# Kernel optimization log

Measured on AMD Instinct MI355X. Metric: run time of the kernel, lower is better.

## Reference

```python
import jax, jax.numpy as jnp
import numpy as np
import math

B, CIN, H, W = 32, 128, 64, 64
COUT, KH, KW = 256, 3, 3


def setup_inputs() -> dict:
    key = jax.random.key(0)
    k1, k2, k3 = jax.random.split(key, 3)
    sqrtk = math.sqrt(1.0 / (CIN * KH * KW))
    x = jax.random.normal(k1, (B, CIN, H, W), dtype=jnp.float32)
    weight = jax.random.uniform(k2, (COUT, CIN, KH, KW), dtype=jnp.float32, minval=-sqrtk, maxval=sqrtk)
    bias = jax.random.uniform(k3, (COUT,), dtype=jnp.float32, minval=-sqrtk, maxval=sqrtk)
    return {"input": x, "weight": weight, "bias": bias}


def reference(input, weight, bias):
    # VALID (no padding), stride-1 cross-correlation conv, NCHW/OIHW layout,
    # matching the original nested-loop direct convolution + per-channel bias.
    out = jax.lax.conv_general_dilated(
        input, weight,
        window_strides=(1, 1), padding='VALID',
        dimension_numbers=('NCHW', 'OIHW', 'NCHW'))
    return out + bias[None, :, None, None]
```

## Files before the change

kernel.cpp:

```cpp
#include <hip/hip_runtime.h>

#define NB   32
#define NCI  128
#define NH   64
#define NW   64
#define NCO  256
#define NOH  62
#define NOW  62

typedef __attribute__((ext_vector_type(8))) short bf16x8;
typedef __attribute__((ext_vector_type(8))) unsigned short u16x8;
typedef __attribute__((ext_vector_type(4))) float f32x4;

typedef __attribute__((address_space(1))) const unsigned int glb_u32_t;
typedef __attribute__((address_space(3))) unsigned int lds_u32_t;

__device__ __forceinline__ unsigned short f2bf(float f) {
  unsigned int u = __float_as_uint(f);
  u = u + 0x7FFFu + ((u >> 16) & 1u);
  return (unsigned short)(u >> 16);
}

__device__ __forceinline__ void gload_lds16(const unsigned short* g, unsigned short* l) {
  __builtin_amdgcn_global_load_lds((glb_u32_t*)g, (lds_u32_t*)l, 16, 0, 0);
}

__global__ __launch_bounds__(256) void cvt_x_kernel(const float* __restrict__ x,
                                                    unsigned short* __restrict__ xt) {
  __shared__ unsigned short l[64 * 130];
  const int tid = threadIdx.x;
  const int b = blockIdx.x >> 6, h = blockIdx.x & 63;
  const int w0 = tid & 63, c0 = tid >> 6;
  const float* src = x + ((size_t)b * NCI * NH + h) * NW;
  #pragma unroll
  for (int g = 0; g < 32; ++g) {
    int ci = g * 4 + c0;
    l[w0 * 130 + ci] = f2bf(src[(size_t)ci * (NH * NW) + w0]);
  }
  __syncthreads();
  unsigned short* dst = xt + ((size_t)b * NH + h) * NW * NCI;
  #pragma unroll
  for (int it = 0; it < 4; ++it) {
    int gidx = it * 2048 + tid * 8;
    int w = gidx >> 7, ci0 = gidx & 127;
    const unsigned int* lw = (const unsigned int*)(l + w * 130 + ci0);
    union { u16x8 v; unsigned int u[4]; } t;
    t.u[0] = lw[0]; t.u[1] = lw[1]; t.u[2] = lw[2]; t.u[3] = lw[3];
    *(u16x8*)(dst + w * NCI + ci0) = t.v;
  }
}

__global__ __launch_bounds__(256) void cvt_w_kernel(const float* __restrict__ wsrc,
                                                    unsigned short* __restrict__ wt) {
  int t = blockIdx.x * 256 + threadIdx.x;
  int oc = t & 15, co = (t >> 4) & 255, k = t >> 12;
  const float* src = wsrc + ((size_t)co * NCI + oc * 8) * 9 + k;
  u16x8 v;
  #pragma unroll
  for (int j = 0; j < 8; ++j) v[j] = f2bf(src[j * 9]);
  *(u16x8*)(wt + ((size_t)k * NCO + co) * NCI + oc * 8) = v;
}

__global__ __launch_bounds__(256, 2) void conv_mfma_kernel(
    const unsigned short* __restrict__ xt, const unsigned short* __restrict__ wt,
    const float* __restrict__ bias, float* __restrict__ out) {
  __shared__ unsigned short smem[40960];

  const int tid  = threadIdx.x;
  const int lane = tid & 63;
  const int wid  = tid >> 6;
  const int wn   = wid;
  const int l15  = lane & 15;
  const int lo   = lane >> 4;

  const int bid0  = blockIdx.x;
  const int bid   = (bid0 & 7) * 128 + (bid0 >> 3);
  const int coutg = bid & 1;
  const int ohg   = (bid >> 1) & 15;
  const int b     = bid >> 5;
  const int cbase = coutg * 128;
  const int oh0   = ohg * 4;

  f32x4 acc[8][4];
  #pragma unroll
  for (int mi = 0; mi < 8; ++mi)
    #pragma unroll
    for (int ni = 0; ni < 4; ++ni)
      acc[mi][ni] = (f32x4){0.f, 0.f, 0.f, 0.f};

  const char* sm = (const char*)smem;
  const int af_lane = l15 * 64 + ((lo ^ ((l15 >> 1) & 3)) << 4);

  const size_t xbase = (size_t)b * NH * NW * NCI;
  const unsigned short* xsrc[6];
  #pragma unroll
  for (int i = 0; i < 6; ++i) {
    int e = (wid * 6 + i) * 64 + lane;
    int o = e & 3, w = (e >> 2) & 63, r = e >> 8;
    int row = oh0 + r; if (row > 63) row = 63;
    xsrc[i] = xt + xbase + ((size_t)row * NW + w) * NCI
            + ((o ^ ((w >> 1) & 3)) * 8);
  }
  const unsigned short* wsrc2[2];
  #pragma unroll
  for (int i = 0; i < 2; ++i) {
    int e = (wid * 2 + i) * 64 + lane;
    int o = e & 3, co = e >> 2;
    wsrc2[i] = wt + (size_t)(cbase + co) * NCI + ((o ^ ((co >> 1) & 3)) * 8);
  }

  auto stage_w = [&](int t) {
    unsigned short* dst = smem + 24576 + (t & 3) * 4096;
    const size_t so = (size_t)(t % 9) * NCO * NCI + (t / 9) * 32;
    #pragma unroll
    for (int i = 0; i < 2; ++i)
      gload_lds16(wsrc2[i] + so, dst + ((wid * 2 + i) * 64 + lane) * 8);
  };
  auto stage_x = [&](int c) {
    unsigned short* dst = smem + (c & 1) * 12288;
    #pragma unroll
    for (int i = 0; i < 6; ++i)
      gload_lds16(xsrc[i] + c * 32, dst + ((wid * 6 + i) * 64 + lane) * 8);
  };

  stage_w(0);
  stage_w(1);
  stage_x(0);
  asm volatile("s_waitcnt vmcnt(0)" ::: "memory");
  __builtin_amdgcn_s_barrier();
  __builtin_amdgcn_sched_barrier(0);

  for (int t = 0; t < 36; ++t) {
    const int t9 = t % 9, c = t / 9;
    const int kh = t9 / 3, kw = t9 - kh * 3;

    const char* wsp = sm + 49152 + (t & 3) * 8192;
    const char* xsp = sm + (c & 1) * 24576 + (wn + kh) * 4096;
    const int w9  = l15 + kw;
    const int bfl = w9 * 64 + ((lo ^ ((w9 >> 1) & 3)) << 4);
    bf16x8 af[8], bfv[4];
    #pragma unroll
    for (int mi = 0; mi < 8; ++mi)
      af[mi] = *(const bf16x8*)(wsp + mi * 1024 + af_lane);
    #pragma unroll
    for (int ni = 0; ni < 4; ++ni)
      bfv[ni] = *(const bf16x8*)(xsp + ni * 1024 + bfl);

    if (t + 2 < 36) stage_w(t + 2);
    const bool xstage = (t9 == 3) && (c < 3);
    if (xstage) stage_x(c + 1);

    __builtin_amdgcn_sched_barrier(0);
    if (t >= 34) {
      asm volatile("s_waitcnt vmcnt(0)" ::: "memory");
    } else if (xstage || (t9 == 4 && c < 3)) {
      asm volatile("s_waitcnt vmcnt(8)" ::: "memory");
    } else {
      asm volatile("s_waitcnt vmcnt(2)" ::: "memory");
    }
    __builtin_amdgcn_s_barrier();
    asm volatile("s_waitcnt lgkmcnt(0)" ::: "memory");
    __builtin_amdgcn_sched_barrier(0);

    __builtin_amdgcn_s_setprio(1);
    #pragma unroll
    for (int mi = 0; mi < 8; ++mi)
      #pragma unroll
      for (int ni = 0; ni < 4; ++ni)
        acc[mi][ni] = __builtin_amdgcn_mfma_f32_16x16x32_bf16(
            af[mi], bfv[ni], acc[mi][ni], 0, 0, 0);
    __builtin_amdgcn_s_setprio(0);
  }

  const int oh = oh0 + wn;
  if (oh < NOH) {
    #pragma unroll
    for (int mi = 0; mi < 8; ++mi) {
      int co0 = cbase + mi * 16 + lo * 4;
      const f32x4 bv = *(const f32x4*)(bias + co0);
      #pragma unroll
      for (int ni = 0; ni < 4; ++ni) {
        int ow = ni * 16 + l15;
        if (ow < NOW) {
          size_t o0 = (((size_t)b * NCO + co0) * NOH + oh) * NOW + ow;
          const size_t cs = (size_t)NOH * NOW;
          out[o0]          = acc[mi][ni][0] + bv[0];
          out[o0 + cs]     = acc[mi][ni][1] + bv[1];
          out[o0 + 2 * cs] = acc[mi][ni][2] + bv[2];
          out[o0 + 3 * cs] = acc[mi][ni][3] + bv[3];
        }
      }
    }
  }
}

__global__ __launch_bounds__(256) void conv_naive_kernel(
    const float* __restrict__ x, const float* __restrict__ w,
    const float* __restrict__ bias, float* __restrict__ out) {
  long t = (long)blockIdx.x * 256 + threadIdx.x;
  const long total = (long)NB * NCO * NOH * NOW;
  if (t >= total) return;
  int ow = (int)(t % NOW);
  int oh = (int)((t / NOW) % NOH);
  int co = (int)((t / ((long)NOW * NOH)) % NCO);
  int b  = (int)(t / ((long)NOW * NOH * NCO));
  float acc = bias[co];
  for (int ci = 0; ci < NCI; ++ci) {
    const float* xp = x + (((size_t)b * NCI + ci) * NH + oh) * NW + ow;
    const float* wp = w + ((size_t)co * NCI + ci) * 9;
    #pragma unroll
    for (int kh = 0; kh < 3; ++kh)
      #pragma unroll
      for (int kw = 0; kw < 3; ++kw)
        acc += xp[kh * NW + kw] * wp[kh * 3 + kw];
  }
  out[t] = acc;
}

extern "C" void kernel_launch(void* const* d_in, const int* in_sizes, int n_in,
                              void* d_out, int out_size, void* d_ws, size_t ws_size,
                              hipStream_t stream) {
  const float* x    = (const float*)d_in[0];
  const float* w    = (const float*)d_in[1];
  const float* bias = (const float*)d_in[2];
  float* out        = (float*)d_out;

  const size_t WT_BYTES = (size_t)9 * NCO * NCI * 2;
  const size_t XT_BYTES = (size_t)NB * NH * NW * NCI * 2;

  if (ws_size >= WT_BYTES + XT_BYTES) {
    unsigned short* wt = (unsigned short*)d_ws;
    unsigned short* xt = (unsigned short*)((char*)d_ws + WT_BYTES);
    cvt_w_kernel<<<(9 * NCO * 16) / 256, 256, 0, stream>>>(w, wt);
    cvt_x_kernel<<<NB * NH, 256, 0, stream>>>(x, xt);
    conv_mfma_kernel<<<2 * 16 * NB, 256, 0, stream>>>(xt, wt, bias, out);
  } else {
    const long total = (long)NB * NCO * NOH * NOW;
    conv_naive_kernel<<<(int)((total + 255) / 256), 256, 0, stream>>>(x, w, bias, out);
  }
}
```

Measured before the change: 97.85 us.

## Process two conv taps per barrier and overlap LDS reads with MFMA

The main loop now handles two of the 36 (channel-chunk, kernel-tap) steps per iteration, so the wait and barrier run once per pair instead of once per step. Weight staging is grouped into paired double buffers, and the global-to-LDS loads for the next pair are issued right after the barrier. The second tap's weight fragments are read from LDS between the MFMA batches, so those reads can overlap with matrix work. In exchange, vmcnt waits are mostly full drains, which can leave less prefetch distance, and holding fragments for both taps raises register pressure against the two-blocks-per-CU occupancy target.

```diff
diff --git a/kernel.cpp b/kernel.cpp
--- a/kernel.cpp
+++ b/kernel.cpp
@@ -110,7 +110,7 @@
   }
 
   auto stage_w = [&](int t) {
-    unsigned short* dst = smem + 24576 + (t & 3) * 4096;
+    unsigned short* dst = smem + 24576 + ((t >> 1) & 1) * 8192 + (t & 1) * 4096;
     const size_t so = (size_t)(t % 9) * NCO * NCI + (t / 9) * 32;
     #pragma unroll
     for (int i = 0; i < 2; ++i)
@@ -126,49 +126,72 @@
   stage_w(0);
   stage_w(1);
   stage_x(0);
-  asm volatile("s_waitcnt vmcnt(0)" ::: "memory");
-  __builtin_amdgcn_s_barrier();
-  __builtin_amdgcn_sched_barrier(0);
-
-  for (int t = 0; t < 36; ++t) {
-    const int t9 = t % 9, c = t / 9;
-    const int kh = t9 / 3, kw = t9 - kh * 3;
-
-    const char* wsp = sm + 49152 + (t & 3) * 8192;
-    const char* xsp = sm + (c & 1) * 24576 + (wn + kh) * 4096;
-    const int w9  = l15 + kw;
-    const int bfl = w9 * 64 + ((lo ^ ((w9 >> 1) & 3)) << 4);
-    bf16x8 af[8], bfv[4];
-    #pragma unroll
-    for (int mi = 0; mi < 8; ++mi)
-      af[mi] = *(const bf16x8*)(wsp + mi * 1024 + af_lane);
-    #pragma unroll
-    for (int ni = 0; ni < 4; ++ni)
-      bfv[ni] = *(const bf16x8*)(xsp + ni * 1024 + bfl);
-
-    if (t + 2 < 36) stage_w(t + 2);
-    const bool xstage = (t9 == 3) && (c < 3);
-    if (xstage) stage_x(c + 1);
-
-    __builtin_amdgcn_sched_barrier(0);
-    if (t >= 34) {
+
+  for (int k = 0; k < 18; ++k) {
+    const int ta = 2 * k, tb = ta + 1;
+    const int t9a = ta % 9, caa = ta / 9;
+    const int t9b = tb % 9, cbb = tb / 9;
+    const int kha = t9a / 3, kwa = t9a - kha * 3;
+    const int khb = t9b / 3, kwb = t9b - khb * 3;
+
+    if (k == 2 || k == 7 || k == 11) {
+      asm volatile("s_waitcnt vmcnt(6)" ::: "memory");
+    } else {
       asm volatile("s_waitcnt vmcnt(0)" ::: "memory");
-    } else if (xstage || (t9 == 4 && c < 3)) {
-      asm volatile("s_waitcnt vmcnt(8)" ::: "memory");
-    } else {
-      asm volatile("s_waitcnt vmcnt(2)" ::: "memory");
     }
     __builtin_amdgcn_s_barrier();
-    asm volatile("s_waitcnt lgkmcnt(0)" ::: "memory");
     __builtin_amdgcn_sched_barrier(0);
 
+    if (ta + 2 < 36) stage_w(ta + 2);
+    if (tb + 2 < 36) stage_w(tb + 2);
+    if (k == 1) stage_x(1);
+    else if (k == 6) stage_x(2);
+    else if (k == 10) stage_x(3);
+
+    const char* wspg = sm + 49152 + (k & 1) * 16384;
+    const char* xspa = sm + (caa & 1) * 24576 + (wn + kha) * 4096;
+    const char* xspb = sm + (cbb & 1) * 24576 + (wn + khb) * 4096;
+    const int w9a = l15 + kwa;
+    const int bfla = w9a * 64 + ((lo ^ ((w9a >> 1) & 3)) << 4);
+    const int w9b = l15 + kwb;
+    const int bflb = w9b * 64 + ((lo ^ ((w9b >> 1) & 3)) << 4);
+
+    bf16x8 afA[8], bfA[4], afB[8], bfB[4];
+    #pragma unroll
+    for (int mi = 0; mi < 8; ++mi)
+      afA[mi] = *(const bf16x8*)(wspg + mi * 1024 + af_lane);
+    #pragma unroll
+    for (int ni = 0; ni < 4; ++ni)
+      bfA[ni] = *(const bf16x8*)(xspa + ni * 1024 + bfla);
+    #pragma unroll
+    for (int ni = 0; ni < 4; ++ni)
+      bfB[ni] = *(const bf16x8*)(xspb + ni * 1024 + bflb);
+
     __builtin_amdgcn_s_setprio(1);
     #pragma unroll
-    for (int mi = 0; mi < 8; ++mi)
+    for (int mi = 0; mi < 4; ++mi)
       #pragma unroll
       for (int ni = 0; ni < 4; ++ni)
         acc[mi][ni] = __builtin_amdgcn_mfma_f32_16x16x32_bf16(
-            af[mi], bfv[ni], acc[mi][ni], 0, 0, 0);
+            afA[mi], bfA[ni], acc[mi][ni], 0, 0, 0);
+
+    #pragma unroll
+    for (int mi = 0; mi < 8; ++mi)
+      afB[mi] = *(const bf16x8*)(wspg + 8192 + mi * 1024 + af_lane);
+
+    #pragma unroll
+    for (int mi = 4; mi < 8; ++mi)
+      #pragma unroll
+      for (int ni = 0; ni < 4; ++ni)
+        acc[mi][ni] = __builtin_amdgcn_mfma_f32_16x16x32_bf16(
+            afA[mi], bfA[ni], acc[mi][ni], 0, 0, 0);
+
+    #pragma unroll
+    for (int mi = 0; mi < 8; ++mi)
+      #pragma unroll
+      for (int ni = 0; ni < 4; ++ni)
+        acc[mi][ni] = __builtin_amdgcn_mfma_f32_16x16x32_bf16(
+            afB[mi], bfB[ni], acc[mi][ni], 0, 0, 0);
     __builtin_amdgcn_s_setprio(0);
   }
 
```

New measurement: 96.46 us. No clear change (-1.4%).

## Double-buffer MFMA fragments and interleave next-tap LDS reads with MFMAs

Applied to the files above, without the earlier changes.

Restructures the 36-tap main loop into a 4x-unrolled schedule with two register fragment sets. LDS reads for the next tap are issued between the current tap's MFMA groups, so LDS latency hides behind matrix math instead of stalling each iteration. The weight prefetch depth goes from two taps to three using the 4-slot ring. This needs more VGPRs for the second fragment set and retunes the vmcnt/barrier schedule by hand, which risks races or lower occupancy.

```diff
diff --git a/kernel.cpp b/kernel.cpp
--- a/kernel.cpp
+++ b/kernel.cpp
@@ -123,53 +123,95 @@
       gload_lds16(xsrc[i] + c * 32, dst + ((wid * 6 + i) * 64 + lane) * 8);
   };
 
+  bf16x8 afA[8], bfA[4], afB[8], bfB[4];
+
+  auto read_frags = [&](bf16x8 (&af)[8], bf16x8 (&bf)[4], int t) {
+    const char* wsp = sm + 49152 + (t & 3) * 8192;
+    const int t9 = t % 9, c = t / 9, kh = t9 / 3, kw = t9 - kh * 3;
+    const char* xsp = sm + (c & 1) * 24576 + (wn + kh) * 4096;
+    const int w9 = l15 + kw;
+    const int bfl = w9 * 64 + ((lo ^ ((w9 >> 1) & 3)) << 4);
+    #pragma unroll
+    for (int mi = 0; mi < 8; ++mi)
+      af[mi] = *(const bf16x8*)(wsp + mi * 1024 + af_lane);
+    #pragma unroll
+    for (int ni = 0; ni < 4; ++ni)
+      bf[ni] = *(const bf16x8*)(xsp + ni * 1024 + bfl);
+  };
+
+  auto tap_mfma = [&](bf16x8 (&caf)[8], bf16x8 (&cbf)[4],
+                      bf16x8 (&naf)[8], bf16x8 (&nbf)[4], int tn, bool pf) {
+    const char* wspn = sm + 49152 + (tn & 3) * 8192;
+    const int t9 = tn % 9, cc = tn / 9, khn = t9 / 3, kwn = t9 - khn * 3;
+    const char* xspn = sm + (cc & 1) * 24576 + (wn + khn) * 4096;
+    const int w9 = l15 + kwn;
+    const int bfln = w9 * 64 + ((lo ^ ((w9 >> 1) & 3)) << 4);
+
+    asm volatile("s_waitcnt lgkmcnt(0)" ::: "memory");
+    __builtin_amdgcn_sched_barrier(0);
+    __builtin_amdgcn_s_setprio(1);
+    #pragma unroll
+    for (int mi = 0; mi < 8; ++mi) {
+      #pragma unroll
+      for (int ni = 0; ni < 4; ++ni)
+        acc[mi][ni] = __builtin_amdgcn_mfma_f32_16x16x32_bf16(
+            caf[mi], cbf[ni], acc[mi][ni], 0, 0, 0);
+      if (pf) {
+        if (mi < 4) {
+          naf[2 * mi]     = *(const bf16x8*)(wspn + (2 * mi) * 1024 + af_lane);
+          naf[2 * mi + 1] = *(const bf16x8*)(wspn + (2 * mi + 1) * 1024 + af_lane);
+        } else if (mi < 6) {
+          nbf[2 * (mi - 4)]     = *(const bf16x8*)(xspn + (2 * (mi - 4)) * 1024 + bfln);
+          nbf[2 * (mi - 4) + 1] = *(const bf16x8*)(xspn + (2 * (mi - 4) + 1) * 1024 + bfln);
+        }
+      }
+    }
+    __builtin_amdgcn_s_setprio(0);
+  };
+
   stage_w(0);
   stage_w(1);
+  stage_w(2);
   stage_x(0);
   asm volatile("s_waitcnt vmcnt(0)" ::: "memory");
   __builtin_amdgcn_s_barrier();
   __builtin_amdgcn_sched_barrier(0);
-
-  for (int t = 0; t < 36; ++t) {
-    const int t9 = t % 9, c = t / 9;
-    const int kh = t9 / 3, kw = t9 - kh * 3;
-
-    const char* wsp = sm + 49152 + (t & 3) * 8192;
-    const char* xsp = sm + (c & 1) * 24576 + (wn + kh) * 4096;
-    const int w9  = l15 + kw;
-    const int bfl = w9 * 64 + ((lo ^ ((w9 >> 1) & 3)) << 4);
-    bf16x8 af[8], bfv[4];
-    #pragma unroll
-    for (int mi = 0; mi < 8; ++mi)
-      af[mi] = *(const bf16x8*)(wsp + mi * 1024 + af_lane);
-    #pragma unroll
-    for (int ni = 0; ni < 4; ++ni)
-      bfv[ni] = *(const bf16x8*)(xsp + ni * 1024 + bfl);
-
-    if (t + 2 < 36) stage_w(t + 2);
-    const bool xstage = (t9 == 3) && (c < 3);
-    if (xstage) stage_x(c + 1);
-
-    __builtin_amdgcn_sched_barrier(0);
-    if (t >= 34) {
-      asm volatile("s_waitcnt vmcnt(0)" ::: "memory");
-    } else if (xstage || (t9 == 4 && c < 3)) {
-      asm volatile("s_waitcnt vmcnt(8)" ::: "memory");
-    } else {
+  read_frags(afA, bfA, 0);
+
+  for (int j = 0; j < 9; ++j) {
+    const int t0 = 4 * j;
+    const bool xst = (j == 1 || j == 3 || j == 5);
+
+    if (t0 + 3 <= 35) stage_w(t0 + 3);
+    if (xst) stage_x(j / 2 + 1);
+    tap_mfma(afA, bfA, afB, bfB, t0 + 1, true);
+    if (xst) { asm volatile("s_waitcnt vmcnt(8)" ::: "memory"); }
+    else     { asm volatile("s_waitcnt vmcnt(2)" ::: "memory"); }
+    __builtin_amdgcn_s_barrier();
+    __builtin_amdgcn_sched_barrier(0);
+
+    if (t0 + 4 <= 35) stage_w(t0 + 4);
+    tap_mfma(afB, bfB, afA, bfA, t0 + 2, true);
+    if (xst)            { asm volatile("s_waitcnt vmcnt(8)" ::: "memory"); }
+    else if (t0 == 32)  { asm volatile("s_waitcnt vmcnt(0)" ::: "memory"); }
+    else                { asm volatile("s_waitcnt vmcnt(2)" ::: "memory"); }
+    __builtin_amdgcn_s_barrier();
+    __builtin_amdgcn_sched_barrier(0);
+
+    if (t0 + 5 <= 35) stage_w(t0 + 5);
+    tap_mfma(afA, bfA, afB, bfB, t0 + 3, true);
+    if (t0 == 32) { asm volatile("s_waitcnt vmcnt(0)" ::: "memory"); }
+    else          { asm volatile("s_waitcnt vmcnt(2)" ::: "memory"); }
+    __builtin_amdgcn_s_barrier();
+    __builtin_amdgcn_sched_barrier(0);
+
+    if (t0 + 6 <= 35) stage_w(t0 + 6);
+    tap_mfma(afB, bfB, afA, bfA, t0 + 4, j < 8);
+    if (j < 8) {
       asm volatile("s_waitcnt vmcnt(2)" ::: "memory");
+      __builtin_amdgcn_s_barrier();
+      __builtin_amdgcn_sched_barrier(0);
     }
-    __builtin_amdgcn_s_barrier();
-    asm volatile("s_waitcnt lgkmcnt(0)" ::: "memory");
-    __builtin_amdgcn_sched_barrier(0);
-
-    __builtin_amdgcn_s_setprio(1);
-    #pragma unroll
-    for (int mi = 0; mi < 8; ++mi)
-      #pragma unroll
-      for (int ni = 0; ni < 4; ++ni)
-        acc[mi][ni] = __builtin_amdgcn_mfma_f32_16x16x32_bf16(
-            af[mi], bfv[ni], acc[mi][ni], 0, 0, 0);
-    __builtin_amdgcn_s_setprio(0);
   }
 
   const int oh = oh0 + wn;
```

After: 96.12 us. About the same (-1.8%).

## Software-pipeline LDS fragment loads with MFMA and deepen weight staging

Applied to the files above, without the earlier changes.

The tap loop is restructured so that LDS reads of A/B fragments for the next tap are interleaved between MFMA groups of the current tap. Register buffers are double-buffered (afX/afY, bfC/bfD) and the loop is unrolled by four. The weight prefetch distance grows from two taps to three, with x staging and vmcnt waits shifted to match. The aim is to hide LDS latency behind matrix work, at the cost of more registers and a tighter ring buffer whose reuse depends on the barrier placement.

```diff
diff --git a/kernel.cpp b/kernel.cpp
--- a/kernel.cpp
+++ b/kernel.cpp
@@ -123,53 +123,109 @@
       gload_lds16(xsrc[i] + c * 32, dst + ((wid * 6 + i) * 64 + lane) * 8);
   };
 
+  bf16x8 afX[4], afY[4], bfC[4], bfD[4];
+
+  auto tap_body = [&](int t, bf16x8 (&bfc)[4], bf16x8 (&bfn)[4], bool pf) {
+    const int t9 = t % 9, c = t / 9;
+    const bool xst = (t9 == 5) && (c < 3);
+    if (t + 3 < 36) stage_w(t + 3);
+    if (xst) stage_x(c + 1);
+
+    const char* wsp = sm + 49152 + (t & 3) * 8192;
+    const int  tn   = t + 1;
+    const char* wspn = sm + 49152 + (tn & 3) * 8192;
+    const int  tn9 = tn % 9, cn = tn / 9;
+    const int  khn = tn9 / 3, kwn = tn9 - khn * 3;
+    const char* xspn = sm + (cn & 1) * 24576 + (wn + khn) * 4096;
+    const int  w9n  = l15 + kwn;
+    const int  bfln = w9n * 64 + ((lo ^ ((w9n >> 1) & 3)) << 4);
+
+    asm volatile("s_waitcnt lgkmcnt(0)" ::: "memory");
+    __builtin_amdgcn_sched_barrier(0);
+    __builtin_amdgcn_s_setprio(1);
+    #pragma unroll
+    for (int ni = 0; ni < 4; ++ni)
+      acc[0][ni] = __builtin_amdgcn_mfma_f32_16x16x32_bf16(afX[0], bfc[ni], acc[0][ni], 0, 0, 0);
+    afY[0] = *(const bf16x8*)(wsp + 4 * 1024 + af_lane);
+    afY[1] = *(const bf16x8*)(wsp + 5 * 1024 + af_lane);
+    #pragma unroll
+    for (int ni = 0; ni < 4; ++ni)
+      acc[1][ni] = __builtin_amdgcn_mfma_f32_16x16x32_bf16(afX[1], bfc[ni], acc[1][ni], 0, 0, 0);
+    afY[2] = *(const bf16x8*)(wsp + 6 * 1024 + af_lane);
+    afY[3] = *(const bf16x8*)(wsp + 7 * 1024 + af_lane);
+    #pragma unroll
+    for (int ni = 0; ni < 4; ++ni)
+      acc[2][ni] = __builtin_amdgcn_mfma_f32_16x16x32_bf16(afX[2], bfc[ni], acc[2][ni], 0, 0, 0);
+    #pragma unroll
+    for (int ni = 0; ni < 4; ++ni)
+      acc[3][ni] = __builtin_amdgcn_mfma_f32_16x16x32_bf16(afX[3], bfc[ni], acc[3][ni], 0, 0, 0);
+    __builtin_amdgcn_s_setprio(0);
+
+    asm volatile("s_waitcnt lgkmcnt(0)" ::: "memory");
+    __builtin_amdgcn_sched_barrier(0);
+    __builtin_amdgcn_s_setprio(1);
+    #pragma unroll
+    for (int ni = 0; ni < 4; ++ni)
+      acc[4][ni] = __builtin_amdgcn_mfma_f32_16x16x32_bf16(afY[0], bfc[ni], acc[4][ni], 0, 0, 0);
+    if (pf) {
+      afX[0] = *(const bf16x8*)(wspn + 0 * 1024 + af_lane);
+      afX[1] = *(const bf16x8*)(wspn + 1 * 1024 + af_lane);
+    }
+    #pragma unroll
+    for (int ni = 0; ni < 4; ++ni)
+      acc[5][ni] = __builtin_amdgcn_mfma_f32_16x16x32_bf16(afY[1], bfc[ni], acc[5][ni], 0, 0, 0);
+    if (pf) {
+      afX[2] = *(const bf16x8*)(wspn + 2 * 1024 + af_lane);
+      afX[3] = *(const bf16x8*)(wspn + 3 * 1024 + af_lane);
+    }
+    #pragma unroll
+    for (int ni = 0; ni < 4; ++ni)
+      acc[6][ni] = __builtin_amdgcn_mfma_f32_16x16x32_bf16(afY[2], bfc[ni], acc[6][ni], 0, 0, 0);
+    if (pf) {
+      #pragma unroll
+      for (int i = 0; i < 4; ++i)
+        bfn[i] = *(const bf16x8*)(xspn + i * 1024 + bfln);
+    }
+    #pragma unroll
+    for (int ni = 0; ni < 4; ++ni)
+      acc[7][ni] = __builtin_amdgcn_mfma_f32_16x16x32_bf16(afY[3], bfc[ni], acc[7][ni], 0, 0, 0);
+    __builtin_amdgcn_s_setprio(0);
+
+    if (t >= 33) {
+      asm volatile("s_waitcnt vmcnt(0)" ::: "memory");
+    } else if ((t9 == 5 || t9 == 6) && c < 3) {
+      asm volatile("s_waitcnt vmcnt(8)" ::: "memory");
+    } else {
+      asm volatile("s_waitcnt vmcnt(2)" ::: "memory");
+    }
+    __builtin_amdgcn_s_barrier();
+    __builtin_amdgcn_sched_barrier(0);
+  };
+
   stage_w(0);
   stage_w(1);
+  stage_w(2);
   stage_x(0);
   asm volatile("s_waitcnt vmcnt(0)" ::: "memory");
   __builtin_amdgcn_s_barrier();
   __builtin_amdgcn_sched_barrier(0);
-
-  for (int t = 0; t < 36; ++t) {
-    const int t9 = t % 9, c = t / 9;
-    const int kh = t9 / 3, kw = t9 - kh * 3;
-
-    const char* wsp = sm + 49152 + (t & 3) * 8192;
-    const char* xsp = sm + (c & 1) * 24576 + (wn + kh) * 4096;
-    const int w9  = l15 + kw;
-    const int bfl = w9 * 64 + ((lo ^ ((w9 >> 1) & 3)) << 4);
-    bf16x8 af[8], bfv[4];
-    #pragma unroll
-    for (int mi = 0; mi < 8; ++mi)
-      af[mi] = *(const bf16x8*)(wsp + mi * 1024 + af_lane);
-    #pragma unroll
-    for (int ni = 0; ni < 4; ++ni)
-      bfv[ni] = *(const bf16x8*)(xsp + ni * 1024 + bfl);
-
-    if (t + 2 < 36) stage_w(t + 2);
-    const bool xstage = (t9 == 3) && (c < 3);
-    if (xstage) stage_x(c + 1);
-
-    __builtin_amdgcn_sched_barrier(0);
-    if (t >= 34) {
-      asm volatile("s_waitcnt vmcnt(0)" ::: "memory");
-    } else if (xstage || (t9 == 4 && c < 3)) {
-      asm volatile("s_waitcnt vmcnt(8)" ::: "memory");
-    } else {
-      asm volatile("s_waitcnt vmcnt(2)" ::: "memory");
-    }
-    __builtin_amdgcn_s_barrier();
-    asm volatile("s_waitcnt lgkmcnt(0)" ::: "memory");
-    __builtin_amdgcn_sched_barrier(0);
-
-    __builtin_amdgcn_s_setprio(1);
-    #pragma unroll
-    for (int mi = 0; mi < 8; ++mi)
-      #pragma unroll
-      for (int ni = 0; ni < 4; ++ni)
-        acc[mi][ni] = __builtin_amdgcn_mfma_f32_16x16x32_bf16(
-            af[mi], bfv[ni], acc[mi][ni], 0, 0, 0);
-    __builtin_amdgcn_s_setprio(0);
+  {
+    const char* wsp0 = sm + 49152;
+    #pragma unroll
+    for (int i = 0; i < 4; ++i)
+      afX[i] = *(const bf16x8*)(wsp0 + i * 1024 + af_lane);
+    const char* xsp0 = sm + wn * 4096;
+    #pragma unroll
+    for (int i = 0; i < 4; ++i)
+      bfC[i] = *(const bf16x8*)(xsp0 + i * 1024 + af_lane);
+  }
+
+  for (int j = 0; j < 9; ++j) {
+    const int t0 = 4 * j;
+    tap_body(t0 + 0, bfC, bfD, true);
+    tap_body(t0 + 1, bfD, bfC, true);
+    tap_body(t0 + 2, bfC, bfD, true);
+    tap_body(t0 + 3, bfD, bfC, j < 8);
   }
 
   const int oh = oh0 + wn;
```

Result: faster. 95.08 us (-2.8%).
